# Kernel tuning notes

Hardware: AMD Instinct MI355X
Metric: run time of the kernel (lower is better)

The kernel has to match this reference:

```python
import jax, jax.numpy as jnp
import numpy as np

B, T, S, E, H = 8, 1024, 1024, 1024, 16
HS = E // H
FF = 4 * E
EPS = 1e-5


def layernorm(x, g, b):
    mu = jnp.mean(x, axis=-1, keepdims=True)
    var = jnp.mean(jnp.square(x - mu), axis=-1, keepdims=True)
    return (x - mu) * jax.lax.rsqrt(var + EPS) * g + b


def mha(q_in, k_in, v_in, Wq, Wk, Wv, Wo, bo, mask4):
    # Wq/Wk/Wv: [E, E] with columns grouped per head (equivalent to the
    # per-head nn.Linear weights concatenated along the output dim).
    Bq, Tq, _ = q_in.shape
    Tk = k_in.shape[1]
    q = (q_in @ Wq).reshape(Bq, Tq, H, HS)
    k = (k_in @ Wk).reshape(Bq, Tk, H, HS)
    v = (v_in @ Wv).reshape(Bq, Tk, H, HS)
    scores = jnp.einsum('bqhd,bkhd->bhqk', q, k) * (HS ** -0.5)
    scores = jnp.where(mask4, scores, -jnp.inf)
    attn = jax.nn.softmax(scores, axis=-1)  # dropout is identity in eval
    out = jnp.einsum('bhqk,bkhd->bqhd', attn, v).reshape(Bq, Tq, E)
    return out @ Wo + bo


def setup_inputs() -> dict:
    key = jax.random.key(0)
    ks = jax.random.split(key, 12)
    sd = E ** -0.5
    inp = {
        'x': jax.random.normal(ks[0], (B, T, E), jnp.float32),
        'enc_out': jax.random.normal(ks[1], (B, S, E), jnp.float32),
        'tgt_mask': jnp.ones((B, T), dtype=bool),
        'src_mask': jnp.ones((B, S), dtype=bool),
        'ln1_g': jnp.ones((E,), jnp.float32), 'ln1_b': jnp.zeros((E,), jnp.float32),
        'ln2_g': jnp.ones((E,), jnp.float32), 'ln2_b': jnp.zeros((E,), jnp.float32),
        'ln3_g': jnp.ones((E,), jnp.float32), 'ln3_b': jnp.zeros((E,), jnp.float32),
        'Wq_s': jax.random.normal(ks[2], (E, E), jnp.float32) * sd,
        'Wk_s': jax.random.normal(ks[3], (E, E), jnp.float32) * sd,
        'Wv_s': jax.random.normal(ks[4], (E, E), jnp.float32) * sd,
        'Wo_s': jax.random.normal(ks[5], (E, E), jnp.float32) * sd,
        'bo_s': jnp.zeros((E,), jnp.float32),
        'Wq_c': jax.random.normal(ks[6], (E, E), jnp.float32) * sd,
        'Wk_c': jax.random.normal(ks[7], (E, E), jnp.float32) * sd,
        'Wv_c': jax.random.normal(ks[8], (E, E), jnp.float32) * sd,
        'Wo_c': jax.random.normal(ks[9], (E, E), jnp.float32) * sd,
        'bo_c': jnp.zeros((E,), jnp.float32),
        'W1': jax.random.normal(ks[10], (E, FF), jnp.float32) * sd,
        'b1': jnp.zeros((FF,), jnp.float32),
        'W2': jax.random.normal(ks[11], (FF, E), jnp.float32) * (FF ** -0.5),
        'b2': jnp.zeros((E,), jnp.float32),
    }
    return inp


def reference(x, enc_out, tgt_mask, src_mask,
              ln1_g, ln1_b, ln2_g, ln2_b, ln3_g, ln3_b,
              Wq_s, Wk_s, Wv_s, Wo_s, bo_s,
              Wq_c, Wk_c, Wv_c, Wo_c, bo_c,
              W1, b1, W2, b2):
    Tq = x.shape[1]
    # vectorized equivalent of the Python double-loop: causal AND key-padding
    causal = jnp.tril(jnp.ones((Tq, Tq), dtype=bool))  # [T,T]
    self_mask = (tgt_mask[:, None, :] & causal[None])[:, None, :, :]  # [B,1,T,T]
    cross_mask = src_mask[:, None, None, :]  # [B,1,1,S] broadcasts to [B,H,T,S]

    h1 = layernorm(x, ln1_g, ln1_b)
    x = x + mha(h1, h1, h1, Wq_s, Wk_s, Wv_s, Wo_s, bo_s, self_mask)
    h2 = layernorm(x, ln2_g, ln2_b)
    x = x + mha(h2, enc_out, enc_out, Wq_c, Wk_c, Wv_c, Wo_c, bo_c, cross_mask)
    h3 = layernorm(x, ln3_g, ln3_b)
    ff = jax.nn.relu(h3 @ W1 + b1) @ W2 + b2  # dropout identity in eval
    return x + ff
```

## Files before the change

kernel.cpp:

```cpp
#include <hip/hip_runtime.h>

typedef unsigned short u16;
typedef __attribute__((ext_vector_type(8))) short bf16x8;
typedef __attribute__((ext_vector_type(4))) float f32x4;

__device__ __forceinline__ float bf2f(u16 u) {
    return __uint_as_float(((unsigned)u) << 16);
}
__device__ __forceinline__ u16 f2bf(float f) {
    unsigned u = __float_as_uint(f);
    u = (u + 0x7fffu + ((u >> 16) & 1u)) >> 16;
    return (u16)u;
}
__device__ __forceinline__ u16 f2bf_fast(float f) {
    return (u16)((__float_as_uint(f) + 0x8000u) >> 16);
}
__device__ __forceinline__ float fexp2(float x) { return __builtin_amdgcn_exp2f(x); }
__device__ __forceinline__ void gld_lds16(const u16* g, u16* l) {
    __builtin_amdgcn_global_load_lds(
        (const __attribute__((address_space(1))) void*)g,
        (__attribute__((address_space(3))) void*)l, 16, 0, 0);
}
__device__ __forceinline__ unsigned lds_off(const u16* p) {
    return (unsigned)(unsigned long long)(const __attribute__((address_space(3))) u16*)p;
}
__device__ __forceinline__ void barrier_() {
    asm volatile("" ::: "memory");
    __builtin_amdgcn_s_barrier();
    asm volatile("" ::: "memory");
}
#define VMCNT(n) asm volatile("s_waitcnt vmcnt(" #n ")" ::: "memory")
#define LGKM0() do { \
    asm volatile("s_waitcnt lgkmcnt(0)" ::: "memory"); \
    __builtin_amdgcn_sched_barrier(0); \
} while(0)
#define DSR(dst, addr) asm volatile("ds_read_b128 %0, %1" : "=v"(dst) : "v"(addr))

__global__ __launch_bounds__(256) void convert_f32_bf16(
    const float* __restrict__ in, u16* __restrict__ out) {
    long i = ((long)blockIdx.x * 256 + threadIdx.x) * 4;
    float4 v = *(const float4*)&in[i];
    alignas(8) u16 o[4] = {f2bf(v.x), f2bf(v.y), f2bf(v.z), f2bf(v.w)};
    *(uint2*)&out[i] = *(const uint2*)o;
}

__global__ __launch_bounds__(256) void copy_f32(
    const float* __restrict__ in, float* __restrict__ out) {
    long i = ((long)blockIdx.x * 256 + threadIdx.x) * 4;
    *(float4*)&out[i] = *(const float4*)&in[i];
}

__device__ __forceinline__ void transpose_w_body(
    const float* __restrict__ in, u16* __restrict__ out, int R, int C) {
    __shared__ u16 tile[64][72];
    int r0 = blockIdx.y * 64, c0 = blockIdx.x * 64;
    int tid = threadIdx.x;
#pragma unroll
    for (int it = 0; it < 4; ++it) {
        int f = it * 1024 + tid * 4;
        int r = f >> 6, c = f & 63;
        float4 v = *(const float4*)&in[(long)(r0 + r) * C + (c0 + c)];
        alignas(8) u16 o[4] = {f2bf(v.x), f2bf(v.y), f2bf(v.z), f2bf(v.w)};
        *(uint2*)&tile[r][c] = *(const uint2*)o;
    }
    __syncthreads();
#pragma unroll
    for (int it = 0; it < 2; ++it) {
        int f = it * 2048 + tid * 8;
        int rr = f >> 6, cc = f & 63;
        alignas(16) u16 tmp[8];
#pragma unroll
        for (int i = 0; i < 8; ++i) tmp[i] = tile[cc + i][rr];
        *(uint4*)&out[(long)(c0 + rr) * R + (r0 + cc)] = *(const uint4*)tmp;
    }
}

__global__ __launch_bounds__(256) void transpose_w(
    const float* __restrict__ in, u16* __restrict__ out, int R, int C) {
    transpose_w_body(in, out, R, C);
}

__global__ __launch_bounds__(256) void transpose_w4(
    const float* __restrict__ p0, const float* __restrict__ p1,
    const float* __restrict__ p2, const float* __restrict__ p3,
    u16* __restrict__ out) {
    int z = blockIdx.z;
    const float* in = (z == 0) ? p0 : (z == 1) ? p1 : (z == 2) ? p2 : p3;
    transpose_w_body(in, out + (long)z * 1024 * 1024, 1024, 1024);
}

__global__ __launch_bounds__(256) void transpose_b(
    const u16* __restrict__ in, u16* __restrict__ out,
    int R, int C, int istride, long ibs, long obs) {
    __shared__ u16 tile[64][72];
    const u16* src = in + (long)blockIdx.z * ibs;
    u16* dst = out + (long)blockIdx.z * obs;
    int r0 = blockIdx.y * 64, c0 = blockIdx.x * 64;
    int tid = threadIdx.x;
#pragma unroll
    for (int it = 0; it < 2; ++it) {
        int f = it * 2048 + tid * 8;
        int r = f >> 6, c = f & 63;
        *(uint4*)&tile[r][c] = *(const uint4*)&src[(long)(r0 + r) * istride + (c0 + c)];
    }
    __syncthreads();
#pragma unroll
    for (int it = 0; it < 2; ++it) {
        int f = it * 2048 + tid * 8;
        int rr = f >> 6, cc = f & 63;
        alignas(16) u16 tmp[8];
#pragma unroll
        for (int i = 0; i < 8; ++i) tmp[i] = tile[cc + i][rr];
        *(uint4*)&dst[(long)(c0 + rr) * R + (r0 + cc)] = *(const uint4*)tmp;
    }
}

__global__ __launch_bounds__(256) void ln_kernel(
    const float* __restrict__ x, const float* __restrict__ g,
    const float* __restrict__ bta, u16* __restrict__ y) {
    long row = blockIdx.x;
    int tid = threadIdx.x;
    float4 v4 = *(const float4*)&x[row * 1024 + tid * 4];
    float v[4] = {v4.x, v4.y, v4.z, v4.w};
    float s = 0.f, ss = 0.f;
#pragma unroll
    for (int i = 0; i < 4; ++i) { s += v[i]; ss += v[i] * v[i]; }
#pragma unroll
    for (int o = 1; o < 64; o <<= 1) { s += __shfl_xor(s, o, 64); ss += __shfl_xor(ss, o, 64); }
    __shared__ float red[8];
    int wv = tid >> 6, lane = tid & 63;
    if (lane == 0) { red[wv] = s; red[4 + wv] = ss; }
    __syncthreads();
    s = red[0] + red[1] + red[2] + red[3];
    ss = red[4] + red[5] + red[6] + red[7];
    float mean = s * (1.f / 1024.f);
    float var = ss * (1.f / 1024.f) - mean * mean;
    float rs = rsqrtf(var + 1e-5f);
    float4 g4 = *(const float4*)&g[tid * 4];
    float4 b4 = *(const float4*)&bta[tid * 4];
    float gg[4] = {g4.x, g4.y, g4.z, g4.w};
    float bb[4] = {b4.x, b4.y, b4.z, b4.w};
    alignas(8) u16 o4[4];
#pragma unroll
    for (int i = 0; i < 4; ++i)
        o4[i] = f2bf((v[i] - mean) * rs * gg[i] + bb[i]);
    *(uint2*)&y[row * 1024 + tid * 4] = *(const uint2*)o4;
}

#define STA(b,t,h) do { \
    gld_lds16(Ag + ((h)*128 +  0) * (long)K + (t)*64, AsL + (b)*16384 + (h)*8192); \
    gld_lds16(Ag + ((h)*128 + 64) * (long)K + (t)*64, AsL + (b)*16384 + (h)*8192 + 4096); \
} while(0)
#define STB(b,t,h) do { \
    gld_lds16(Bg + ((h)*128 +  0) * (long)K + (t)*64, BsL + (b)*16384 + (h)*8192); \
    gld_lds16(Bg + ((h)*128 + 64) * (long)K + (t)*64, BsL + (b)*16384 + (h)*8192 + 4096); \
} while(0)
#define RDB(b) do { \
    DSR(bfr[0][0], aB0 + (b)*32768 +    0); DSR(bfr[0][1], aB1 + (b)*32768 +    0); \
    DSR(bfr[1][0], aB0 + (b)*32768 + 2048); DSR(bfr[1][1], aB1 + (b)*32768 + 2048); \
    DSR(bfr[2][0], aB0 + (b)*32768 + 4096); DSR(bfr[2][1], aB1 + (b)*32768 + 4096); \
    DSR(bfr[3][0], aB0 + (b)*32768 + 6144); DSR(bfr[3][1], aB1 + (b)*32768 + 6144); \
} while(0)
#define RDA(b,q) do { \
    DSR(a0, aA0 + (b)*32768 + (2*(q)  )*2048); \
    DSR(a1, aA1 + (b)*32768 + (2*(q)  )*2048); \
    DSR(a2, aA0 + (b)*32768 + (2*(q)+1)*2048); \
    DSR(a3, aA1 + (b)*32768 + (2*(q)+1)*2048); \
} while(0)
#define MM(q) do { \
    __builtin_amdgcn_s_setprio(1); \
    _Pragma("unroll") \
    for (int j = 0; j < 4; ++j) { \
        acc[2*(q)  ][j] = __builtin_amdgcn_mfma_f32_16x16x32_bf16(a0, bfr[j][0], acc[2*(q)  ][j], 0, 0, 0); \
        acc[2*(q)  ][j] = __builtin_amdgcn_mfma_f32_16x16x32_bf16(a1, bfr[j][1], acc[2*(q)  ][j], 0, 0, 0); \
        acc[2*(q)+1][j] = __builtin_amdgcn_mfma_f32_16x16x32_bf16(a2, bfr[j][0], acc[2*(q)+1][j], 0, 0, 0); \
        acc[2*(q)+1][j] = __builtin_amdgcn_mfma_f32_16x16x32_bf16(a3, bfr[j][1], acc[2*(q)+1][j], 0, 0, 0); } \
    __builtin_amdgcn_s_setprio(0); \
} while(0)

template<int BIAS, int RES, int RELU, int OUTF32, int SPLITK>
__device__ __forceinline__ void gemm256_body(
    const u16* __restrict__ A, const u16* __restrict__ Bt,
    const float* __restrict__ bias, const float* __restrict__ res,
    void* __restrict__ Cv, long bm, long bn, int K, int kLen, int koff,
    int ldc, int kz, u16* As, u16* Bs) {
    int tid = threadIdx.x;
    int lane = tid & 63;
    int l15 = lane & 15, quad = lane >> 4;
    int wv = tid >> 6, wm = wv >> 2, wn = wv & 3;
    int NT = kLen >> 6, NI = NT >> 1;

    int srow = tid >> 3;
    int scol = ((tid & 7) ^ (srow & 7)) << 3;
    const u16* Ag = A + (bm + srow) * (long)K + koff + scol;
    const u16* Bg = Bt + (bn + srow) * (long)K + koff + scol;
    u16* AsL = As + tid * 8;
    u16* BsL = Bs + tid * 8;

    int c0 = (quad * 8) ^ ((l15 & 7) << 3);
    int c1 = (32 + quad * 8) ^ ((l15 & 7) << 3);
    unsigned arB = lds_off(As + (wm * 128 + l15) * 64);
    unsigned brB = lds_off(Bs + (wn * 64 + l15) * 64);
    unsigned aA0 = arB + 2 * c0, aA1 = arB + 2 * c1;
    unsigned aB0 = brB + 2 * c0, aB1 = brB + 2 * c1;

    f32x4 zf = {0.f, 0.f, 0.f, 0.f};
    f32x4 acc[8][4];
#pragma unroll
    for (int i = 0; i < 8; ++i)
#pragma unroll
        for (int j = 0; j < 4; ++j) acc[i][j] = zf;

    STA(0,0,0); STA(0,0,1); STB(0,0,0); STB(0,0,1); STB(1,1,0); STB(1,1,1);
    VMCNT(4);
    barrier_();

    bf16x8 bfr[4][2];
    bf16x8 a0, a1, a2, a3;

#pragma unroll 1
    for (int it2 = 0; it2 < NI; ++it2) {
        int t = 2 * it2, t1 = t + 1;
        int ts2 = (t + 2 < NT) ? t + 2 : t;
        int ts3 = (t + 3 < NT) ? t + 3 : t1;
        RDB(0); RDA(0,0); STA(1,t1,0);            barrier_(); LGKM0(); MM(0); barrier_();
        RDA(0,1);         STA(1,t1,1);            barrier_(); LGKM0(); MM(1); barrier_();
        RDA(0,2);         STB(0,ts2,0);           barrier_(); LGKM0(); MM(2); barrier_();
        RDA(0,3);         STB(0,ts2,1); VMCNT(4); barrier_(); LGKM0(); MM(3); barrier_();
        RDB(1); RDA(1,0); STA(0,ts2,0);           barrier_(); LGKM0(); MM(0); barrier_();
        RDA(1,1);         STA(0,ts2,1);           barrier_(); LGKM0(); MM(1); barrier_();
        RDA(1,2);         STB(1,ts3,0);           barrier_(); LGKM0(); MM(2); barrier_();
        RDA(1,3);         STB(1,ts3,1); VMCNT(4); barrier_(); LGKM0(); MM(3); barrier_();
    }
    VMCNT(0);

    long row0 = bm + wm * 128 + quad * 4;
    long col0 = bn + wn * 64 + l15;
#pragma unroll
    for (int i = 0; i < 8; ++i) {
        long row = row0 + i * 16;
#pragma unroll
        for (int j = 0; j < 4; ++j) {
            long col = col0 + j * 16;
            float bv = (BIAS && (!SPLITK || kz == 0)) ? bias[col] : 0.f;
#pragma unroll
            for (int r = 0; r < 4; ++r) {
                float v = acc[i][j][r] + bv;
                if (RES) v += res[(row + r) * ldc + col];
                if (RELU) v = fmaxf(v, 0.f);
                if (SPLITK) atomicAdd(&((float*)Cv)[(row + r) * ldc + col], v);
                else if (OUTF32) ((float*)Cv)[(row + r) * ldc + col] = v;
                else ((u16*)Cv)[(row + r) * ldc + col] = f2bf(v);
            }
        }
    }
}

template<int BIAS, int RES, int RELU, int OUTF32, int SPLITK>
__global__ __launch_bounds__(512) void gemm256(
    const u16* __restrict__ A, const u16* __restrict__ Bt,
    const float* __restrict__ bias, const float* __restrict__ res,
    void* __restrict__ Cv, int tilesM, int K, int ldc) {
    __shared__ u16 As[2 * 256 * 64];
    __shared__ u16 Bs[2 * 256 * 64];
    int id = blockIdx.x;
    long bm = (long)(id % tilesM) * 256, bn = (long)(id / tilesM) * 256;
    int kLen = SPLITK ? (K >> 1) : K;
    int koff = SPLITK ? ((int)blockIdx.y * kLen) : 0;
    gemm256_body<BIAS, RES, RELU, OUTF32, SPLITK>(
        A, Bt, bias, res, Cv, bm, bn, K, kLen, koff, ldc, blockIdx.y, As, Bs);
}

__global__ __launch_bounds__(512) void gemm256_cross(
    const u16* __restrict__ hq, const u16* __restrict__ encb,
    const u16* __restrict__ wT, u16* __restrict__ qbuf, u16* __restrict__ kv) {
    __shared__ u16 As[2 * 256 * 64];
    __shared__ u16 Bs[2 * 256 * 64];
    int id = blockIdx.x;
    const u16* A; const u16* Bt; u16* C; int ldc;
    if (id < 128) { A = hq; Bt = wT; C = qbuf; ldc = 1024; }
    else { id -= 128; A = encb; Bt = wT + 1024l * 1024l; C = kv; ldc = 2048; }
    long bm = (long)(id % 32) * 256, bn = (long)(id / 32) * 256;
    gemm256_body<0, 0, 0, 0, 0>(
        A, Bt, nullptr, nullptr, C, bm, bn, 1024, 1024, 0, ldc, 0, As, Bs);
}

template<bool CAUSAL>
__global__ __launch_bounds__(256) void attn_kernel(
    const u16* __restrict__ q, const u16* __restrict__ k,
    const u16* __restrict__ vT, u16* __restrict__ out, int qld, int kld) {
    __shared__ u16 Qs[64][72];
    __shared__ u16 Ks[64][72];
    __shared__ u16 VTs[64][72];
    __shared__ u16 Ps[4][16][72];
    const int S_ = 1024;
    int qt = CAUSAL ? (gridDim.x - 1 - blockIdx.x) : blockIdx.x;
    int h = blockIdx.y, b = blockIdx.z;
    int tid = threadIdx.x, lane = tid & 63, wv = tid >> 6;
    int l15 = lane & 15, quad = lane >> 4;
    long qbase = ((long)b * 1024 + qt * 64) * qld + h * 64;
    long obase = ((long)b * 1024 + qt * 64) * 1024 + h * 64;
#pragma unroll
    for (int it = 0; it < 2; ++it) {
        int f = it * 2048 + tid * 8;
        int r = f >> 6, c = f & 63;
        *(uint4*)&Qs[r][c] = *(const uint4*)&q[qbase + (long)r * qld + c];
    }
    __syncthreads();
    bf16x8 a0 = *(const bf16x8*)&Qs[wv * 16 + l15][quad * 8];
    bf16x8 a1 = *(const bf16x8*)&Qs[wv * 16 + l15][quad * 8 + 32];
    f32x4 zf = {0.f, 0.f, 0.f, 0.f};
    f32x4 O[4];
#pragma unroll
    for (int j = 0; j < 4; ++j) O[j] = zf;
    const float cs = 0.125f * 1.44269504089f;
    float m_run = -3e30f;
    float lp[4] = {0.f, 0.f, 0.f, 0.f};
    long kbase = (long)b * 1024 * kld + h * 64;
    long vtbase = ((long)b * 16 + h) * 64 * (long)S_;
    int ktmax = CAUSAL ? qt : (S_ / 64 - 1);

    for (int kt = 0; kt <= ktmax; ++kt) {
        __syncthreads();
#pragma unroll
        for (int it = 0; it < 2; ++it) {
            int f = it * 2048 + tid * 8;
            int r = f >> 6, c = f & 63;
            *(uint4*)&Ks[r][c]  = *(const uint4*)&k[kbase + (long)(kt * 64 + r) * kld + c];
            *(uint4*)&VTs[r][c] = *(const uint4*)&vT[vtbase + (long)r * S_ + kt * 64 + c];
        }
        __syncthreads();

        f32x4 s[4];
#pragma unroll
        for (int j = 0; j < 4; ++j) {
            bf16x8 kb0 = *(const bf16x8*)&Ks[j * 16 + l15][quad * 8];
            bf16x8 kb1 = *(const bf16x8*)&Ks[j * 16 + l15][quad * 8 + 32];
            f32x4 z = zf;
            z = __builtin_amdgcn_mfma_f32_16x16x32_bf16(a0, kb0, z, 0, 0, 0);
            z = __builtin_amdgcn_mfma_f32_16x16x32_bf16(a1, kb1, z, 0, 0, 0);
            s[j] = z;
        }
        if (CAUSAL && kt == qt) {
#pragma unroll
            for (int j = 0; j < 4; ++j)
#pragma unroll
                for (int r = 0; r < 4; ++r)
                    if ((j * 16 + l15) > (wv * 16 + quad * 4 + r)) s[j][r] = -3e30f;
        }
        float mx = s[0][0];
#pragma unroll
        for (int j = 0; j < 4; ++j)
#pragma unroll
            for (int r = 0; r < 4; ++r) mx = fmaxf(mx, s[j][r]);
#pragma unroll
        for (int o = 1; o < 64; o <<= 1) mx = fmaxf(mx, __shfl_xor(mx, o, 64));
        float mn = fmaxf(m_run, mx);
        bool grew = mn > m_run;
        if (grew) {
            float alpha = fexp2((m_run - mn) * cs);
            m_run = mn;
#pragma unroll
            for (int j = 0; j < 4; ++j) {
                O[j][0] *= alpha; O[j][1] *= alpha; O[j][2] *= alpha; O[j][3] *= alpha;
            }
#pragma unroll
            for (int r = 0; r < 4; ++r) lp[r] *= alpha;
        }
        float mc = m_run * cs;
#pragma unroll
        for (int j = 0; j < 4; ++j)
#pragma unroll
            for (int r = 0; r < 4; ++r) {
                float p = fexp2(__builtin_fmaf(s[j][r], cs, -mc));
                lp[r] += p;
                Ps[wv][quad * 4 + r][j * 16 + l15] = f2bf_fast(p);
            }
        bf16x8 pa0 = *(const bf16x8*)&Ps[wv][l15][quad * 8];
        bf16x8 pa1 = *(const bf16x8*)&Ps[wv][l15][quad * 8 + 32];
#pragma unroll
        for (int j = 0; j < 4; ++j) {
            bf16x8 vb0 = *(const bf16x8*)&VTs[j * 16 + l15][quad * 8];
            bf16x8 vb1 = *(const bf16x8*)&VTs[j * 16 + l15][quad * 8 + 32];
            f32x4 o = O[j];
            o = __builtin_amdgcn_mfma_f32_16x16x32_bf16(pa0, vb0, o, 0, 0, 0);
            o = __builtin_amdgcn_mfma_f32_16x16x32_bf16(pa1, vb1, o, 0, 0, 0);
            O[j] = o;
        }
    }
#pragma unroll
    for (int r = 0; r < 4; ++r) {
#pragma unroll
        for (int o = 1; o < 16; o <<= 1) lp[r] += __shfl_xor(lp[r], o, 64);
        lp[r] = 1.f / lp[r];
    }
#pragma unroll
    for (int j = 0; j < 4; ++j)
#pragma unroll
        for (int r = 0; r < 4; ++r)
            out[obase + (long)(wv * 16 + quad * 4 + r) * 1024 + j * 16 + l15] =
                f2bf(O[j][r] * lp[r]);
}

extern "C" void kernel_launch(void* const* d_in, const int* in_sizes, int n_in,
                              void* d_out, int out_size, void* d_ws, size_t ws_size,
                              hipStream_t stream) {
    (void)in_sizes; (void)n_in; (void)out_size; (void)ws_size;
    const float* x    = (const float*)d_in[0];
    const float* enc  = (const float*)d_in[1];
    const float* ln1g = (const float*)d_in[4];
    const float* ln1b = (const float*)d_in[5];
    const float* ln2g = (const float*)d_in[6];
    const float* ln2b = (const float*)d_in[7];
    const float* ln3g = (const float*)d_in[8];
    const float* ln3b = (const float*)d_in[9];
    const float* Wq_s = (const float*)d_in[10];
    const float* Wk_s = (const float*)d_in[11];
    const float* Wv_s = (const float*)d_in[12];
    const float* Wo_s = (const float*)d_in[13];
    const float* bo_s = (const float*)d_in[14];
    const float* Wq_c = (const float*)d_in[15];
    const float* Wk_c = (const float*)d_in[16];
    const float* Wv_c = (const float*)d_in[17];
    const float* Wo_c = (const float*)d_in[18];
    const float* bo_c = (const float*)d_in[19];
    const float* W1   = (const float*)d_in[20];
    const float* b1   = (const float*)d_in[21];
    const float* W2   = (const float*)d_in[22];
    const float* b2   = (const float*)d_in[23];
    float* out = (float*)d_out;

    const long MEG = 1024l * 1024l;
    u16* ws0  = (u16*)d_ws;
    u16* hbuf = ws0 + 0 * MEG;
    u16* qkv  = ws0 + 8 * MEG;
    u16* qbuf = ws0 + 8 * MEG;
    u16* kv   = ws0 + 16 * MEG;
    u16* vTb  = ws0 + 32 * MEG;
    u16* encb = ws0 + 32 * MEG;
    u16* wT   = ws0 + 40 * MEG;
    u16* wT3  = ws0 + 43 * MEG;
    float* x1 = (float*)(ws0 + 44 * MEG);
    u16* ff1  = qkv;
    u16* w1T  = ws0 + 44 * MEG;
    u16* w2T  = ws0 + 48 * MEG;

    dim3 blk(256);
    dim3 blk5(512);
    dim3 gW4(16, 16, 4);
    dim3 gA(16, 16, 8);

    transpose_w4<<<gW4, blk, 0, stream>>>(Wq_s, Wk_s, Wv_s, Wo_s, wT);
    ln_kernel<<<8192, blk, 0, stream>>>(x, ln1g, ln1b, hbuf);
    gemm256<0,0,0,0,0><<<384, blk5, 0, stream>>>(hbuf, wT, nullptr, nullptr, qkv, 32, 1024, 3072);
    transpose_b<<<gA, blk, 0, stream>>>(qkv + 2048, vTb, 1024, 1024, 3072, 1024l * 3072, MEG);
    attn_kernel<true><<<gA, blk, 0, stream>>>(qkv, qkv + 1024, vTb, hbuf, 3072, 3072);
    copy_f32<<<8192, blk, 0, stream>>>(x, x1);
    gemm256<1,0,0,1,1><<<dim3(128, 2), blk5, 0, stream>>>(hbuf, wT3, bo_s, nullptr, x1, 32, 1024, 1024);

    transpose_w4<<<gW4, blk, 0, stream>>>(Wq_c, Wk_c, Wv_c, Wo_c, wT);
    ln_kernel<<<8192, blk, 0, stream>>>(x1, ln2g, ln2b, hbuf);
    convert_f32_bf16<<<8192, blk, 0, stream>>>(enc, encb);
    gemm256_cross<<<384, blk5, 0, stream>>>(hbuf, encb, wT, qbuf, kv);
    transpose_b<<<gA, blk, 0, stream>>>(kv + 1024, vTb, 1024, 1024, 2048, 1024l * 2048, MEG);
    attn_kernel<false><<<gA, blk, 0, stream>>>(qbuf, kv, vTb, hbuf, 1024, 2048);
    copy_f32<<<8192, blk, 0, stream>>>(x1, out);
    gemm256<1,0,0,1,1><<<dim3(128, 2), blk5, 0, stream>>>(hbuf, wT3, bo_c, nullptr, out, 32, 1024, 1024);

    transpose_w<<<dim3(64, 16, 1), blk, 0, stream>>>(W1, w1T, 1024, 4096);
    transpose_w<<<dim3(16, 64, 1), blk, 0, stream>>>(W2, w2T, 4096, 1024);
    ln_kernel<<<8192, blk, 0, stream>>>(out, ln3g, ln3b, hbuf);
    gemm256<1,0,1,0,0><<<512, blk5, 0, stream>>>(hbuf, w1T, b1, nullptr, ff1, 32, 1024, 4096);
    gemm256<1,0,0,1,1><<<dim3(128, 2), blk5, 0, stream>>>(ff1, w2T, b2, nullptr, out, 32, 4096, 1024);
}
```

Before: 820.3 us.

## Double-buffer A fragments in GEMM loop and fuse residual into output projections

The GEMM main loop now reads A fragments for the next quarter-step into a second register set and waits with a partial lgkmcnt, so LDS reads overlap the MFMA work of the current step. The MFMA order is also regrouped so that consecutive instructions hit different accumulators. Separately, the two attention output projections drop the copy-plus-split-K-atomic scheme and instead run a non-split GEMM that adds the residual in its epilogue. That removes two copy kernels and the atomics, but halves the grid of those GEMMs (128 blocks) and adds register pressure from the extra fragment registers.

New measurement: 756.9 us. -7.7%, faster.

```diff
diff --git a/kernel.cpp b/kernel.cpp
--- a/kernel.cpp
+++ b/kernel.cpp
@@ -30,8 +30,8 @@
     asm volatile("" ::: "memory");
 }
 #define VMCNT(n) asm volatile("s_waitcnt vmcnt(" #n ")" ::: "memory")
-#define LGKM0() do { \
-    asm volatile("s_waitcnt lgkmcnt(0)" ::: "memory"); \
+#define LGKM(n) do { \
+    asm volatile("s_waitcnt lgkmcnt(" #n ")" ::: "memory"); \
     __builtin_amdgcn_sched_barrier(0); \
 } while(0)
 #define DSR(dst, addr) asm volatile("ds_read_b128 %0, %1" : "=v"(dst) : "v"(addr))
@@ -42,12 +42,6 @@
     float4 v = *(const float4*)&in[i];
     alignas(8) u16 o[4] = {f2bf(v.x), f2bf(v.y), f2bf(v.z), f2bf(v.w)};
     *(uint2*)&out[i] = *(const uint2*)o;
-}
-
-__global__ __launch_bounds__(256) void copy_f32(
-    const float* __restrict__ in, float* __restrict__ out) {
-    long i = ((long)blockIdx.x * 256 + threadIdx.x) * 4;
-    *(float4*)&out[i] = *(const float4*)&in[i];
 }
 
 __device__ __forceinline__ void transpose_w_body(
@@ -161,20 +155,32 @@
     DSR(bfr[2][0], aB0 + (b)*32768 + 4096); DSR(bfr[2][1], aB1 + (b)*32768 + 4096); \
     DSR(bfr[3][0], aB0 + (b)*32768 + 6144); DSR(bfr[3][1], aB1 + (b)*32768 + 6144); \
 } while(0)
-#define RDA(b,q) do { \
-    DSR(a0, aA0 + (b)*32768 + (2*(q)  )*2048); \
-    DSR(a1, aA1 + (b)*32768 + (2*(q)  )*2048); \
-    DSR(a2, aA0 + (b)*32768 + (2*(q)+1)*2048); \
-    DSR(a3, aA1 + (b)*32768 + (2*(q)+1)*2048); \
-} while(0)
-#define MM(q) do { \
+#define RDAP(b,q) do { \
+    DSR(pa0, aA0 + (b)*32768 + (2*(q)  )*2048); \
+    DSR(pa1, aA1 + (b)*32768 + (2*(q)  )*2048); \
+    DSR(pa2, aA0 + (b)*32768 + (2*(q)+1)*2048); \
+    DSR(pa3, aA1 + (b)*32768 + (2*(q)+1)*2048); \
+} while(0)
+#define RDAQ(b,q) do { \
+    DSR(pb0, aA0 + (b)*32768 + (2*(q)  )*2048); \
+    DSR(pb1, aA1 + (b)*32768 + (2*(q)  )*2048); \
+    DSR(pb2, aA0 + (b)*32768 + (2*(q)+1)*2048); \
+    DSR(pb3, aA1 + (b)*32768 + (2*(q)+1)*2048); \
+} while(0)
+#define MM(q, A0, A1, A2, A3) do { \
     __builtin_amdgcn_s_setprio(1); \
     _Pragma("unroll") \
-    for (int j = 0; j < 4; ++j) { \
-        acc[2*(q)  ][j] = __builtin_amdgcn_mfma_f32_16x16x32_bf16(a0, bfr[j][0], acc[2*(q)  ][j], 0, 0, 0); \
-        acc[2*(q)  ][j] = __builtin_amdgcn_mfma_f32_16x16x32_bf16(a1, bfr[j][1], acc[2*(q)  ][j], 0, 0, 0); \
-        acc[2*(q)+1][j] = __builtin_amdgcn_mfma_f32_16x16x32_bf16(a2, bfr[j][0], acc[2*(q)+1][j], 0, 0, 0); \
-        acc[2*(q)+1][j] = __builtin_amdgcn_mfma_f32_16x16x32_bf16(a3, bfr[j][1], acc[2*(q)+1][j], 0, 0, 0); } \
+    for (int j = 0; j < 4; ++j) \
+        acc[2*(q)  ][j] = __builtin_amdgcn_mfma_f32_16x16x32_bf16(A0, bfr[j][0], acc[2*(q)  ][j], 0, 0, 0); \
+    _Pragma("unroll") \
+    for (int j = 0; j < 4; ++j) \
+        acc[2*(q)+1][j] = __builtin_amdgcn_mfma_f32_16x16x32_bf16(A2, bfr[j][0], acc[2*(q)+1][j], 0, 0, 0); \
+    _Pragma("unroll") \
+    for (int j = 0; j < 4; ++j) \
+        acc[2*(q)  ][j] = __builtin_amdgcn_mfma_f32_16x16x32_bf16(A1, bfr[j][1], acc[2*(q)  ][j], 0, 0, 0); \
+    _Pragma("unroll") \
+    for (int j = 0; j < 4; ++j) \
+        acc[2*(q)+1][j] = __builtin_amdgcn_mfma_f32_16x16x32_bf16(A3, bfr[j][1], acc[2*(q)+1][j], 0, 0, 0); \
     __builtin_amdgcn_s_setprio(0); \
 } while(0)
 
@@ -216,21 +222,30 @@
     barrier_();
 
     bf16x8 bfr[4][2];
-    bf16x8 a0, a1, a2, a3;
+    bf16x8 pa0, pa1, pa2, pa3;
+    bf16x8 pb0, pb1, pb2, pb3;
 
 #pragma unroll 1
     for (int it2 = 0; it2 < NI; ++it2) {
         int t = 2 * it2, t1 = t + 1;
         int ts2 = (t + 2 < NT) ? t + 2 : t;
         int ts3 = (t + 3 < NT) ? t + 3 : t1;
-        RDB(0); RDA(0,0); STA(1,t1,0);            barrier_(); LGKM0(); MM(0); barrier_();
-        RDA(0,1);         STA(1,t1,1);            barrier_(); LGKM0(); MM(1); barrier_();
-        RDA(0,2);         STB(0,ts2,0);           barrier_(); LGKM0(); MM(2); barrier_();
-        RDA(0,3);         STB(0,ts2,1); VMCNT(4); barrier_(); LGKM0(); MM(3); barrier_();
-        RDB(1); RDA(1,0); STA(0,ts2,0);           barrier_(); LGKM0(); MM(0); barrier_();
-        RDA(1,1);         STA(0,ts2,1);           barrier_(); LGKM0(); MM(1); barrier_();
-        RDA(1,2);         STB(1,ts3,0);           barrier_(); LGKM0(); MM(2); barrier_();
-        RDA(1,3);         STB(1,ts3,1); VMCNT(4); barrier_(); LGKM0(); MM(3); barrier_();
+        RDB(0); RDAP(0,0); RDAQ(0,1); STA(1,t1,0);
+            barrier_(); LGKM(4); MM(0, pa0,pa1,pa2,pa3); barrier_();
+        RDAP(0,2); STA(1,t1,1);
+            barrier_(); LGKM(4); MM(1, pb0,pb1,pb2,pb3); barrier_();
+        RDAQ(0,3); STB(0,ts2,0);
+            barrier_(); LGKM(4); MM(2, pa0,pa1,pa2,pa3); barrier_();
+        STB(0,ts2,1); VMCNT(4);
+            barrier_(); LGKM(0); MM(3, pb0,pb1,pb2,pb3); barrier_();
+        RDB(1); RDAP(1,0); RDAQ(1,1); STA(0,ts2,0);
+            barrier_(); LGKM(4); MM(0, pa0,pa1,pa2,pa3); barrier_();
+        RDAP(1,2); STA(0,ts2,1);
+            barrier_(); LGKM(4); MM(1, pb0,pb1,pb2,pb3); barrier_();
+        RDAQ(1,3); STB(1,ts3,0);
+            barrier_(); LGKM(4); MM(2, pa0,pa1,pa2,pa3); barrier_();
+        STB(1,ts3,1); VMCNT(4);
+            barrier_(); LGKM(0); MM(3, pb0,pb1,pb2,pb3); barrier_();
     }
     VMCNT(0);
 
@@ -455,8 +470,7 @@
     gemm256<0,0,0,0,0><<<384, blk5, 0, stream>>>(hbuf, wT, nullptr, nullptr, qkv, 32, 1024, 3072);
     transpose_b<<<gA, blk, 0, stream>>>(qkv + 2048, vTb, 1024, 1024, 3072, 1024l * 3072, MEG);
     attn_kernel<true><<<gA, blk, 0, stream>>>(qkv, qkv + 1024, vTb, hbuf, 3072, 3072);
-    copy_f32<<<8192, blk, 0, stream>>>(x, x1);
-    gemm256<1,0,0,1,1><<<dim3(128, 2), blk5, 0, stream>>>(hbuf, wT3, bo_s, nullptr, x1, 32, 1024, 1024);
+    gemm256<1,1,0,1,0><<<128, blk5, 0, stream>>>(hbuf, wT3, bo_s, x, x1, 32, 1024, 1024);
 
     transpose_w4<<<gW4, blk, 0, stream>>>(Wq_c, Wk_c, Wv_c, Wo_c, wT);
     ln_kernel<<<8192, blk, 0, stream>>>(x1, ln2g, ln2b, hbuf);
@@ -464,8 +478,7 @@
     gemm256_cross<<<384, blk5, 0, stream>>>(hbuf, encb, wT, qbuf, kv);
     transpose_b<<<gA, blk, 0, stream>>>(kv + 1024, vTb, 1024, 1024, 2048, 1024l * 2048, MEG);
     attn_kernel<false><<<gA, blk, 0, stream>>>(qbuf, kv, vTb, hbuf, 1024, 2048);
-    copy_f32<<<8192, blk, 0, stream>>>(x1, out);
-    gemm256<1,0,0,1,1><<<dim3(128, 2), blk5, 0, stream>>>(hbuf, wT3, bo_c, nullptr, out, 32, 1024, 1024);
+    gemm256<1,1,0,1,0><<<128, blk5, 0, stream>>>(hbuf, wT3, bo_c, x1, out, 32, 1024, 1024);
 
     transpose_w<<<dim3(64, 16, 1), blk, 0, stream>>>(W1, w1T, 1024, 4096);
     transpose_w<<<dim3(16, 64, 1), blk, 0, stream>>>(W2, w2T, 4096, 1024);
```
